# Performance work log

Measured on AMD Instinct MI355X. Metric: run time of the kernel, lower is better.

## Reference

```python
import jax, jax.numpy as jnp
import numpy as np

DIM = 768
N_HEADS = 12
HEAD_DIM = DIM // N_HEADS
B, S = 16, 1024


def setup_inputs() -> dict:
    key = jax.random.key(0)
    k1, k2, k3, k4, k5 = jax.random.split(key, 5)
    scale = 0.02
    return {
        "x": jax.random.normal(k1, (B, S, DIM), dtype=jnp.float32),
        "W_attn": jax.random.normal(k2, (DIM, 3 * DIM), dtype=jnp.float32) * scale,
        "b_attn": jnp.zeros((3 * DIM,), dtype=jnp.float32),
        "W_proj": jax.random.normal(k3, (DIM, DIM), dtype=jnp.float32) * scale,
        "b_proj": jnp.zeros((DIM,), dtype=jnp.float32),
    }


def reference(x, W_attn, b_attn, W_proj, b_proj):
    # Dropout layers act as identity (eval mode) for a deterministic reference.
    Bsz, Sq, D = x.shape
    qkv = x @ W_attn + b_attn                      # [B, S, 3D]
    q, k, v = jnp.split(qkv, 3, axis=-1)
    q = q.reshape(Bsz, Sq, N_HEADS, HEAD_DIM)
    k = k.reshape(Bsz, Sq, N_HEADS, HEAD_DIM)
    v = v.reshape(Bsz, Sq, N_HEADS, HEAD_DIM)
    # scores: [B, H, S, S]
    w = jnp.einsum('bqhd,bkhd->bhqk', q, k) / jnp.sqrt(jnp.float32(HEAD_DIM))
    causal = jnp.tril(jnp.ones((Sq, Sq), dtype=bool))
    mask_value = jnp.finfo(w.dtype).min
    w = jnp.where(causal[None, None], w, mask_value)
    w = jax.nn.softmax(w, axis=-1)
    attn = jnp.einsum('bhqk,bkhd->bqhd', w, v).reshape(Bsz, Sq, D)
    return attn @ W_proj + b_proj
```

## Files before the change

### kernel.cpp

```cpp
#include <hip/hip_runtime.h>
#include <hip/hip_bf16.h>
#include <math.h>

#define BDIM 16
#define SEQ 1024
#define DIM 768
#define NH 12
#define HD 64
#define M_ROWS (BDIM * SEQ)
#define N_QKV (3 * DIM)
#define QN (BDIM * NH * SEQ * HD)

typedef __attribute__((ext_vector_type(8))) short bf16x8_t;
typedef __attribute__((ext_vector_type(4))) float f32x4_t;
typedef __attribute__((ext_vector_type(16))) float f32x16_t;
typedef __attribute__((ext_vector_type(4))) unsigned int u32x4_t;

__device__ __forceinline__ unsigned short f2bf(float x) {
    return __builtin_bit_cast(unsigned short, __float2bfloat16(x));
}

__device__ __forceinline__ void gld_lds16(const void* g, void* l) {
    __builtin_amdgcn_global_load_lds(
        (const __attribute__((address_space(1))) void*)g,
        (__attribute__((address_space(3))) void*)l, 16, 0, 0);
}

__device__ __forceinline__ unsigned int cvt_pk_bf16(float a, float b) {
    unsigned int r;
    asm("v_cvt_pk_bf16_f32 %0, %1, %2" : "=v"(r) : "v"(a), "v"(b));
    return r;
}

__device__ __forceinline__ void perm32swap(unsigned int& a, unsigned int& b) {
    asm("v_permlane32_swap_b32 %0, %1" : "+v"(a), "+v"(b));
}

__device__ __forceinline__ float exp2_fast(float x) {
    float r;
    asm("v_exp_f32 %0, %1" : "=v"(r) : "v"(x));
    return r;
}

__device__ __forceinline__ int xcd_remap(int lin, int chunk) {
    return (lin & 7) * chunk + (lin >> 3);
}

#define QSCALE 0.18033688011112042f

#define X_BLOCKS 6144
#define WA_TILES 432
#define WP_TILES 144

__global__ __launch_bounds__(256) void prep(
    const float* __restrict__ x, const float* __restrict__ Wa,
    const float* __restrict__ Wp,
    unsigned short* __restrict__ xb, unsigned short* __restrict__ Wat,
    unsigned short* __restrict__ Wpt)
{
    __shared__ unsigned short T[64][72];
    const int bid = blockIdx.x;
    const int tid = threadIdx.x;

    if (bid < X_BLOCKS) {
        size_t base = (size_t)bid * 2048 + tid * 8;
        float4 f0 = *(const float4*)&x[base];
        float4 f1 = *(const float4*)&x[base + 4];
        unsigned short tmp[8] = {f2bf(f0.x), f2bf(f0.y), f2bf(f0.z), f2bf(f0.w),
                                 f2bf(f1.x), f2bf(f1.y), f2bf(f1.z), f2bf(f1.w)};
        *(uint4*)&xb[base] = *(uint4*)tmp;
        return;
    }
    const float* W; unsigned short* Wt; int N, kt, nt;
    int b2 = bid - X_BLOCKS;
    if (b2 < WA_TILES) { W = Wa; Wt = Wat; N = N_QKV; kt = b2 / 36; nt = b2 % 36; }
    else { b2 -= WA_TILES; W = Wp; Wt = Wpt; N = DIM; kt = b2 / 12; nt = b2 % 12; }
    const int k0 = kt * 64, n0 = nt * 64;
#pragma unroll
    for (int c = 0; c < 4; c++) {
        int idx = c * 256 + tid;
        int r = idx >> 4;
        int c4 = (idx & 15) * 4;
        float4 v = *(const float4*)&W[(size_t)(k0 + r) * N + n0 + c4];
        T[r][c4 + 0] = f2bf(v.x);
        T[r][c4 + 1] = f2bf(v.y);
        T[r][c4 + 2] = f2bf(v.z);
        T[r][c4 + 3] = f2bf(v.w);
    }
    __syncthreads();
#pragma unroll
    for (int c = 0; c < 2; c++) {
        int idx = c * 256 + tid;
        int n = idx >> 3;
        int ch = (idx & 7) * 8;
        unsigned short tmp[8];
#pragma unroll
        for (int j = 0; j < 8; j++) tmp[j] = T[ch + j][n];
        *(uint4*)&Wt[(size_t)(n0 + n) * DIM + k0 + ch] = *(uint4*)tmp;
    }
}

__global__ __launch_bounds__(256, 2) void gemm_qkv_mfma(
    const unsigned short* __restrict__ Ab,
    const unsigned short* __restrict__ Bt,
    const float* __restrict__ bias,
    unsigned short* __restrict__ Qo, unsigned short* __restrict__ Ko,
    unsigned short* __restrict__ Vt)
{
    __shared__ unsigned short smem[32768];

    const int tid = threadIdx.x;
    const int lane = tid & 63;
    const int w = tid >> 6;
    const int wm = w >> 1, wn = w & 1;
    const int ln = lane & 15, quad = lane >> 4;
    const int lin = blockIdx.x + 18 * blockIdx.y;
    const int jj = xcd_remap(lin, 288);
    const int bm = (jj / 18) * 128, bn = (jj % 18) * 128;

    f32x4_t acc[4][4];
#pragma unroll
    for (int i = 0; i < 4; i++)
#pragma unroll
        for (int j = 0; j < 4; j++) acc[i][j] = (f32x4_t){0.f, 0.f, 0.f, 0.f};

#pragma unroll
    for (int c = 0; c < 4; c++) {
        int idx = c * 256 + tid;
        int r = idx >> 3;
        int gch = (idx & 7) ^ (r & 7);
        gld_lds16(&Ab[(size_t)(bm + r) * DIM + gch * 8], &smem[idx * 8]);
        gld_lds16(&Bt[(size_t)(bn + r) * DIM + gch * 8], &smem[8192 + idx * 8]);
    }

    for (int ki = 0; ki < 12; ki++) {
        __syncthreads();
        unsigned short* As = smem + (ki & 1) * 16384;
        unsigned short* Bs = As + 8192;

        if (ki < 11) {
            const int nk0 = (ki + 1) * 64;
            unsigned short* Asn = smem + ((ki + 1) & 1) * 16384;
            unsigned short* Bsn = Asn + 8192;
#pragma unroll
            for (int c = 0; c < 4; c++) {
                int idx = c * 256 + tid;
                int r = idx >> 3;
                int gch = (idx & 7) ^ (r & 7);
                gld_lds16(&Ab[(size_t)(bm + r) * DIM + nk0 + gch * 8], &Asn[idx * 8]);
                gld_lds16(&Bt[(size_t)(bn + r) * DIM + nk0 + gch * 8], &Bsn[idx * 8]);
            }
        }

#pragma unroll
        for (int kk = 0; kk < 2; kk++) {
            bf16x8_t af[4], bfr[4];
#pragma unroll
            for (int mt = 0; mt < 4; mt++) {
                int r = wm * 64 + mt * 16 + ln;
                int c = (kk * 4 + quad) ^ (ln & 7);
                af[mt] = *(const bf16x8_t*)&As[r * 64 + c * 8];
            }
#pragma unroll
            for (int nt = 0; nt < 4; nt++) {
                int r = wn * 64 + nt * 16 + ln;
                int c = (kk * 4 + quad) ^ (ln & 7);
                bfr[nt] = *(const bf16x8_t*)&Bs[r * 64 + c * 8];
            }
#pragma unroll
            for (int mt = 0; mt < 4; mt++)
#pragma unroll
                for (int nt = 0; nt < 4; nt++)
                    acc[mt][nt] = __builtin_amdgcn_mfma_f32_16x16x32_bf16(
                        af[mt], bfr[nt], acc[mt][nt], 0, 0, 0);
        }
    }
    __syncthreads();

    const int nb = bn + wn * 64;
    const int part = nb / DIM;
    const int h = (nb % DIM) >> 6;
    const float scale = (part == 0) ? QSCALE : 1.0f;
    const int mb = bm + wm * 64;
    const int b_ = mb >> 10;
    const int s0 = mb & 1023;
    unsigned short* Wb = smem + w * 4608;

    float bias_v[4];
#pragma unroll
    for (int nt = 0; nt < 4; nt++) bias_v[nt] = bias[nb + nt * 16 + ln];

    if (part < 2) {
#pragma unroll
        for (int mt = 0; mt < 4; mt++)
#pragma unroll
            for (int nt = 0; nt < 4; nt++)
#pragma unroll
                for (int r = 0; r < 4; r++)
                    Wb[(mt * 16 + quad * 4 + r) * 72 + nt * 16 + ln] =
                        f2bf((acc[mt][nt][r] + bias_v[nt]) * scale);
        unsigned short* dst = (part == 0) ? Qo : Ko;
        size_t obase = (((size_t)b_ * NH + h) * SEQ + s0) * HD;
#pragma unroll
        for (int c = 0; c < 8; c++) {
            int idx = c * 64 + lane;
            int rr = idx >> 3;
            int ch = (idx & 7) * 8;
            *(uint4*)&dst[obase + (size_t)rr * HD + ch] = *(uint4*)&Wb[rr * 72 + ch];
        }
    } else {
#pragma unroll
        for (int mt = 0; mt < 4; mt++)
#pragma unroll
            for (int nt = 0; nt < 4; nt++)
#pragma unroll
                for (int r = 0; r < 4; r++)
                    Wb[(nt * 16 + ln) * 72 + mt * 16 + quad * 4 + r] =
                        f2bf(acc[mt][nt][r] + bias_v[nt]);
        size_t obase = ((size_t)b_ * NH + h) * (size_t)HD * SEQ;
#pragma unroll
        for (int c = 0; c < 8; c++) {
            int idx = c * 64 + lane;
            int d = idx >> 3;
            int ch = (idx & 7) * 8;
            *(uint4*)&Vt[obase + (size_t)d * SEQ + s0 + ch] = *(uint4*)&Wb[d * 72 + ch];
        }
    }
}

__global__ __launch_bounds__(256, 2) void gemm_proj_mfma(
    const unsigned short* __restrict__ Ab,
    const unsigned short* __restrict__ Bt,
    const float* __restrict__ bias,
    float* __restrict__ C)
{
    __shared__ unsigned short smem[32768];

    const int tid = threadIdx.x;
    const int lane = tid & 63;
    const int w = tid >> 6;
    const int wm = w >> 1, wn = w & 1;
    const int ln = lane & 15, quad = lane >> 4;
    const int lin = blockIdx.x + 6 * blockIdx.y;
    const int jj = xcd_remap(lin, 96);
    const int bm = (jj / 6) * 128, bn = (jj % 6) * 128;

    f32x4_t acc[4][4];
#pragma unroll
    for (int i = 0; i < 4; i++)
#pragma unroll
        for (int j = 0; j < 4; j++) acc[i][j] = (f32x4_t){0.f, 0.f, 0.f, 0.f};

#pragma unroll
    for (int c = 0; c < 4; c++) {
        int idx = c * 256 + tid;
        int r = idx >> 3;
        int gch = (idx & 7) ^ (r & 7);
        gld_lds16(&Ab[(size_t)(bm + r) * DIM + gch * 8], &smem[idx * 8]);
        gld_lds16(&Bt[(size_t)(bn + r) * DIM + gch * 8], &smem[8192 + idx * 8]);
    }

    for (int ki = 0; ki < 12; ki++) {
        __syncthreads();
        unsigned short* As = smem + (ki & 1) * 16384;
        unsigned short* Bs = As + 8192;

        if (ki < 11) {
            const int nk0 = (ki + 1) * 64;
            unsigned short* Asn = smem + ((ki + 1) & 1) * 16384;
            unsigned short* Bsn = Asn + 8192;
#pragma unroll
            for (int c = 0; c < 4; c++) {
                int idx = c * 256 + tid;
                int r = idx >> 3;
                int gch = (idx & 7) ^ (r & 7);
                gld_lds16(&Ab[(size_t)(bm + r) * DIM + nk0 + gch * 8], &Asn[idx * 8]);
                gld_lds16(&Bt[(size_t)(bn + r) * DIM + nk0 + gch * 8], &Bsn[idx * 8]);
            }
        }

#pragma unroll
        for (int kk = 0; kk < 2; kk++) {
            bf16x8_t af[4], bfr[4];
#pragma unroll
            for (int mt = 0; mt < 4; mt++) {
                int r = wm * 64 + mt * 16 + ln;
                int c = (kk * 4 + quad) ^ (ln & 7);
                af[mt] = *(const bf16x8_t*)&As[r * 64 + c * 8];
            }
#pragma unroll
            for (int nt = 0; nt < 4; nt++) {
                int r = wn * 64 + nt * 16 + ln;
                int c = (kk * 4 + quad) ^ (ln & 7);
                bfr[nt] = *(const bf16x8_t*)&Bs[r * 64 + c * 8];
            }
#pragma unroll
            for (int mt = 0; mt < 4; mt++)
#pragma unroll
                for (int nt = 0; nt < 4; nt++)
                    acc[mt][nt] = __builtin_amdgcn_mfma_f32_16x16x32_bf16(
                        af[mt], bfr[nt], acc[mt][nt], 0, 0, 0);
        }
    }

    const int nb = bn + wn * 64;
    float bias_v[4];
#pragma unroll
    for (int nt = 0; nt < 4; nt++) bias_v[nt] = bias[nb + nt * 16 + ln];
#pragma unroll
    for (int mt = 0; mt < 4; mt++)
#pragma unroll
        for (int nt = 0; nt < 4; nt++)
#pragma unroll
            for (int r = 0; r < 4; r++) {
                int m = bm + wm * 64 + mt * 16 + quad * 4 + r;
                C[(size_t)m * DIM + nb + nt * 16 + ln] = acc[mt][nt][r] + bias_v[nt];
            }
}

#define SWZ(r) ((((r) & 7)) ^ ((((r) >> 3)) & 3))

__global__ __launch_bounds__(256, 3) void attn_mfma(
    const unsigned short* __restrict__ Qg, const unsigned short* __restrict__ Kg,
    const unsigned short* __restrict__ Vt, unsigned short* __restrict__ Out)
{
    __shared__ unsigned short Ks[2][4096];
    __shared__ unsigned short Vs[2][4096];

    const int tid = threadIdx.x;
    const int lane = tid & 63;
    const int w = tid >> 6;
    const int wpair = w >> 1;
    const int whigh = w & 1;
    const int l31 = lane & 31;
    const int hi = lane >> 5;
    const int l7 = lane & 7;
    const int sw3 = (l31 >> 3) & 3;

    const int lin = blockIdx.x + 4 * blockIdx.y;
    const int jj = xcd_remap(lin, 96);
    const int bxn = jj & 3;
    const int bh = jj >> 2;
    const size_t gbase = (size_t)bh * SEQ * HD;
    const int b_ = bh / NH;
    const int h = bh % NH;

    bf16x8_t vones;
#pragma unroll
    for (int i = 0; i < 8; i++) vones[i] = (short)0x3F80;

    for (int ph = 0; ph < 2; ph++) {
        const int qt = ph ? bxn : 7 - bxn;
        const int qbase = qt * 128;
        const int ntiles = 2 * qt + 2;
        const int wtiles = 2 * qt + 1 + wpair;
        const int qr0 = qbase + w * 32;

        bf16x8_t aq[4];
#pragma unroll
        for (int ds = 0; ds < 4; ds++)
            aq[ds] = *(const bf16x8_t*)
                &Qg[gbase + (size_t)(qr0 + l31) * HD + ds * 16 + hi * 8];

        f32x16_t acc[2];
        f32x16_t lacc;
#pragma unroll
        for (int j = 0; j < 16; j++) {
            acc[0][j] = 0.f; acc[1][j] = 0.f; lacc[j] = 0.f;
        }

        __syncthreads();

#pragma unroll
        for (int i = 0; i < 2; i++) {
            int idx = i * 256 + tid;
            int r = idx >> 3;
            int gc = (idx & 7) ^ SWZ(r);
            gld_lds16(&Kg[gbase + (size_t)r * HD + gc * 8], &Ks[0][idx * 8]);
            gld_lds16(&Vt[gbase + (size_t)r * SEQ + gc * 8], &Vs[0][idx * 8]);
        }

        for (int t = 0; t < ntiles; t++) {
            __syncthreads();
            const int cur = t & 1;

            if (t + 1 < ntiles) {
                const int nk0 = (t + 1) * 64;
#pragma unroll
                for (int i = 0; i < 2; i++) {
                    int idx = i * 256 + tid;
                    int r = idx >> 3;
                    int gc = (idx & 7) ^ SWZ(r);
                    gld_lds16(&Kg[gbase + (size_t)(nk0 + r) * HD + gc * 8],
                              &Ks[cur ^ 1][idx * 8]);
                    gld_lds16(&Vt[gbase + (size_t)r * SEQ + nk0 + gc * 8],
                              &Vs[cur ^ 1][idx * 8]);
                }
            }
            if (t >= wtiles) continue;
            const bool diag = (t == 2 * qt + wpair);
            const int kgend = diag ? (1 + whigh) : 2;

            for (int kg = 0; kg < kgend; kg++) {
                bf16x8_t kf[4];
#pragma unroll
                for (int ds = 0; ds < 4; ds++)
                    kf[ds] = *(const bf16x8_t*)
                        &Ks[cur][(kg * 32 + l31) * 64 +
                                 (((ds * 2 + hi) ^ l7 ^ sw3) * 8)];

                f32x16_t sa;
#pragma unroll
                for (int j = 0; j < 16; j++) sa[j] = 0.f;
                __builtin_amdgcn_s_setprio(1);
#pragma unroll
                for (int ds = 0; ds < 4; ds++)
                    sa = __builtin_amdgcn_mfma_f32_32x32x16_bf16(
                        kf[ds], aq[ds], sa, 0, 0, 0);
                __builtin_amdgcn_s_setprio(0);

                const bool dm = diag && (kg == whigh);
                const int qr = qr0 + l31;
                float p[16];
#pragma unroll
                for (int j = 0; j < 16; j++) {
                    float pv = exp2_fast(sa[j]);
                    if (dm) {
                        int key = t * 64 + kg * 32 + (j & 3) + 8 * (j >> 2) + 4 * hi;
                        if (key > qr) pv = 0.f;
                    }
                    p[j] = pv;
                }
                unsigned int c0 = cvt_pk_bf16(p[0], p[1]);
                unsigned int c1 = cvt_pk_bf16(p[2], p[3]);
                unsigned int c2 = cvt_pk_bf16(p[4], p[5]);
                unsigned int c3 = cvt_pk_bf16(p[6], p[7]);
                unsigned int c4 = cvt_pk_bf16(p[8], p[9]);
                unsigned int c5 = cvt_pk_bf16(p[10], p[11]);
                unsigned int c6 = cvt_pk_bf16(p[12], p[13]);
                unsigned int c7 = cvt_pk_bf16(p[14], p[15]);
                perm32swap(c0, c2);
                perm32swap(c1, c3);
                perm32swap(c4, c6);
                perm32swap(c5, c7);
                u32x4_t u0, u1;
                u0[0] = c0; u0[1] = c1; u0[2] = c2; u0[3] = c3;
                u1[0] = c4; u1[1] = c5; u1[2] = c6; u1[3] = c7;
                bf16x8_t pa0 = __builtin_bit_cast(bf16x8_t, u0);
                bf16x8_t pa1 = __builtin_bit_cast(bf16x8_t, u1);

                __builtin_amdgcn_s_setprio(1);
                lacc = __builtin_amdgcn_mfma_f32_32x32x16_bf16(
                    pa0, vones, lacc, 0, 0, 0);
                lacc = __builtin_amdgcn_mfma_f32_32x32x16_bf16(
                    pa1, vones, lacc, 0, 0, 0);
#pragma unroll
                for (int dh = 0; dh < 2; dh++) {
                    bf16x8_t vf0 = *(const bf16x8_t*)
                        &Vs[cur][(dh * 32 + l31) * 64 +
                                 (((kg * 4 + 0 + hi) ^ l7 ^ sw3) * 8)];
                    acc[dh] = __builtin_amdgcn_mfma_f32_32x32x16_bf16(
                        pa0, vf0, acc[dh], 0, 0, 0);
                    bf16x8_t vf1 = *(const bf16x8_t*)
                        &Vs[cur][(dh * 32 + l31) * 64 +
                                 (((kg * 4 + 2 + hi) ^ l7 ^ sw3) * 8)];
                    acc[dh] = __builtin_amdgcn_mfma_f32_32x32x16_bf16(
                        pa1, vf1, acc[dh], 0, 0, 0);
                }
                __builtin_amdgcn_s_setprio(0);
            }
        }

        float rin[16];
#pragma unroll
        for (int j = 0; j < 16; j++) rin[j] = 1.0f / lacc[j];
#pragma unroll
        for (int dh = 0; dh < 2; dh++)
#pragma unroll
            for (int j = 0; j < 16; j++) {
                int row = qr0 + (j & 3) + 8 * (j >> 2) + 4 * hi;
                Out[((size_t)b_ * SEQ + row) * DIM + h * HD + dh * 32 + l31] =
                    f2bf(acc[dh][j] * rin[j]);
            }
    }
}

extern "C" void kernel_launch(void* const* d_in, const int* in_sizes, int n_in,
                              void* d_out, int out_size, void* d_ws, size_t ws_size,
                              hipStream_t stream) {
    const float* x  = (const float*)d_in[0];
    const float* Wa = (const float*)d_in[1];
    const float* ba = (const float*)d_in[2];
    const float* Wp = (const float*)d_in[3];
    const float* bp = (const float*)d_in[4];
    float* out = (float*)d_out;

    unsigned short* ws = (unsigned short*)d_ws;
    unsigned short* Qg  = ws;
    unsigned short* Kg  = Qg + (size_t)QN;
    unsigned short* Vt  = Kg + (size_t)QN;
    unsigned short* xb  = Vt + (size_t)QN;
    unsigned short* AO  = xb;
    unsigned short* Wat = xb + (size_t)QN;
    unsigned short* Wpt = Wat + (size_t)(N_QKV * DIM);

    prep<<<X_BLOCKS + WA_TILES + WP_TILES, 256, 0, stream>>>(
        x, Wa, Wp, xb, Wat, Wpt);

    dim3 g_qkv(N_QKV / 128, M_ROWS / 128);
    gemm_qkv_mfma<<<g_qkv, 256, 0, stream>>>(xb, Wat, ba, Qg, Kg, Vt);

    dim3 g_attn(4, BDIM * NH);
    attn_mfma<<<g_attn, 256, 0, stream>>>(Qg, Kg, Vt, AO);

    dim3 g_proj(DIM / 128, M_ROWS / 128);
    gemm_proj_mfma<<<g_proj, 256, 0, stream>>>(AO, Wpt, bp, out);
}
```

Baseline: 239.0 us.

## Enlarge GEMM tiles to 256x256 with 512 threads and deeper prefetch

Both the QKV and projection GEMMs move from 128x128 tiles with 4 waves to 256x256 tiles with 8 waves. Each wave now computes a 128x64 sub-tile, and B fragments are reused across four A sub-steps. Loads are issued two K-steps ahead, using explicit vmcnt waits and s_setprio around the MFMA bursts. This raises data reuse per byte loaded but cuts the grid to 72 and 24 blocks on a many-CU GPU, and the larger LDS footprint limits occupancy.

```diff
diff --git a/kernel.cpp b/kernel.cpp
--- a/kernel.cpp
+++ b/kernel.cpp
@@ -100,206 +100,235 @@
     }
 }
 
-__global__ __launch_bounds__(256, 2) void gemm_qkv_mfma(
+__device__ __forceinline__ void stage_tile256(
+    const unsigned short* __restrict__ Ab, const unsigned short* __restrict__ Bt,
+    int bm, int bn, int k0, unsigned short* Asd, unsigned short* Bsd, int tid)
+{
+#pragma unroll
+    for (int rr = 0; rr < 4; rr++) {
+        int idx = rr * 512 + tid;
+        int r = idx >> 3;
+        int gch = (idx & 7) ^ (r & 7);
+        gld_lds16(&Ab[(size_t)(bm + r) * DIM + k0 + gch * 8], &Asd[idx * 8]);
+    }
+#pragma unroll
+    for (int rr = 0; rr < 4; rr++) {
+        int idx = rr * 512 + tid;
+        int r = idx >> 3;
+        int gch = (idx & 7) ^ (r & 7);
+        gld_lds16(&Bt[(size_t)(bn + r) * DIM + k0 + gch * 8], &Bsd[idx * 8]);
+    }
+}
+
+__global__ __launch_bounds__(512, 2) void gemm_qkv_mfma(
     const unsigned short* __restrict__ Ab,
     const unsigned short* __restrict__ Bt,
     const float* __restrict__ bias,
     unsigned short* __restrict__ Qo, unsigned short* __restrict__ Ko,
     unsigned short* __restrict__ Vt)
 {
-    __shared__ unsigned short smem[32768];
+    __shared__ unsigned short As[2 * 16384];
+    __shared__ unsigned short Bs[2 * 16384];
 
     const int tid = threadIdx.x;
     const int lane = tid & 63;
     const int w = tid >> 6;
-    const int wm = w >> 1, wn = w & 1;
+    const int wm = w >> 2, wn = w & 3;
     const int ln = lane & 15, quad = lane >> 4;
-    const int lin = blockIdx.x + 18 * blockIdx.y;
-    const int jj = xcd_remap(lin, 288);
-    const int bm = (jj / 18) * 128, bn = (jj % 18) * 128;
-
-    f32x4_t acc[4][4];
-#pragma unroll
-    for (int i = 0; i < 4; i++)
+
+    const int lin = blockIdx.x + 9 * blockIdx.y;
+    const int jj = xcd_remap(lin, 72);
+    const int bm = (jj / 9) * 256, bn = (jj % 9) * 256;
+
+    f32x4_t acc[8][4];
+#pragma unroll
+    for (int i = 0; i < 8; i++)
 #pragma unroll
         for (int j = 0; j < 4; j++) acc[i][j] = (f32x4_t){0.f, 0.f, 0.f, 0.f};
 
-#pragma unroll
-    for (int c = 0; c < 4; c++) {
-        int idx = c * 256 + tid;
-        int r = idx >> 3;
-        int gch = (idx & 7) ^ (r & 7);
-        gld_lds16(&Ab[(size_t)(bm + r) * DIM + gch * 8], &smem[idx * 8]);
-        gld_lds16(&Bt[(size_t)(bn + r) * DIM + gch * 8], &smem[8192 + idx * 8]);
-    }
-
-    for (int ki = 0; ki < 12; ki++) {
-        __syncthreads();
-        unsigned short* As = smem + (ki & 1) * 16384;
-        unsigned short* Bs = As + 8192;
-
-        if (ki < 11) {
-            const int nk0 = (ki + 1) * 64;
-            unsigned short* Asn = smem + ((ki + 1) & 1) * 16384;
-            unsigned short* Bsn = Asn + 8192;
-#pragma unroll
-            for (int c = 0; c < 4; c++) {
-                int idx = c * 256 + tid;
-                int r = idx >> 3;
-                int gch = (idx & 7) ^ (r & 7);
-                gld_lds16(&Ab[(size_t)(bm + r) * DIM + nk0 + gch * 8], &Asn[idx * 8]);
-                gld_lds16(&Bt[(size_t)(bn + r) * DIM + nk0 + gch * 8], &Bsn[idx * 8]);
-            }
-        }
-
-#pragma unroll
-        for (int kk = 0; kk < 2; kk++) {
-            bf16x8_t af[4], bfr[4];
-#pragma unroll
-            for (int mt = 0; mt < 4; mt++) {
-                int r = wm * 64 + mt * 16 + ln;
-                int c = (kk * 4 + quad) ^ (ln & 7);
-                af[mt] = *(const bf16x8_t*)&As[r * 64 + c * 8];
-            }
-#pragma unroll
-            for (int nt = 0; nt < 4; nt++) {
+    stage_tile256(Ab, Bt, bm, bn, 0, As, Bs, tid);
+    stage_tile256(Ab, Bt, bm, bn, 64, As + 16384, Bs + 16384, tid);
+    asm volatile("s_waitcnt vmcnt(8)" ::: "memory");
+    __syncthreads();
+
+    for (int k = 0; k < 12; k++) {
+        const unsigned short* As_ = As + (k & 1) * 16384;
+        const unsigned short* Bs_ = Bs + (k & 1) * 16384;
+
+        bf16x8_t bfr[4][2];
+#pragma unroll
+        for (int nt = 0; nt < 4; nt++)
+#pragma unroll
+            for (int kk = 0; kk < 2; kk++) {
                 int r = wn * 64 + nt * 16 + ln;
                 int c = (kk * 4 + quad) ^ (ln & 7);
-                bfr[nt] = *(const bf16x8_t*)&Bs[r * 64 + c * 8];
-            }
-#pragma unroll
-            for (int mt = 0; mt < 4; mt++)
+                bfr[nt][kk] = *(const bf16x8_t*)&Bs_[r * 64 + c * 8];
+            }
+#pragma unroll
+        for (int q = 0; q < 4; q++) {
+            bf16x8_t af[2][2];
+#pragma unroll
+            for (int mi = 0; mi < 2; mi++)
+#pragma unroll
+                for (int kk = 0; kk < 2; kk++) {
+                    int r = wm * 128 + (q * 2 + mi) * 16 + ln;
+                    int c = (kk * 4 + quad) ^ (ln & 7);
+                    af[mi][kk] = *(const bf16x8_t*)&As_[r * 64 + c * 8];
+                }
+            __builtin_amdgcn_s_setprio(1);
+#pragma unroll
+            for (int mi = 0; mi < 2; mi++)
 #pragma unroll
                 for (int nt = 0; nt < 4; nt++)
-                    acc[mt][nt] = __builtin_amdgcn_mfma_f32_16x16x32_bf16(
-                        af[mt], bfr[nt], acc[mt][nt], 0, 0, 0);
-        }
-    }
-    __syncthreads();
+#pragma unroll
+                    for (int kk = 0; kk < 2; kk++)
+                        acc[q * 2 + mi][nt] = __builtin_amdgcn_mfma_f32_16x16x32_bf16(
+                            af[mi][kk], bfr[nt][kk], acc[q * 2 + mi][nt], 0, 0, 0);
+            __builtin_amdgcn_s_setprio(0);
+        }
+
+        __syncthreads();
+        if (k + 2 < 12)
+            stage_tile256(Ab, Bt, bm, bn, (k + 2) * 64,
+                          (unsigned short*)As + (k & 1) * 16384,
+                          (unsigned short*)Bs + (k & 1) * 16384, tid);
+        if (k + 1 < 12) {
+            if (k + 2 < 12) asm volatile("s_waitcnt vmcnt(8)" ::: "memory");
+            else            asm volatile("s_waitcnt vmcnt(0)" ::: "memory");
+            __syncthreads();
+        }
+    }
 
     const int nb = bn + wn * 64;
     const int part = nb / DIM;
     const int h = (nb % DIM) >> 6;
     const float scale = (part == 0) ? QSCALE : 1.0f;
-    const int mb = bm + wm * 64;
+    const int mb = bm + wm * 128;
     const int b_ = mb >> 10;
     const int s0 = mb & 1023;
-    unsigned short* Wb = smem + w * 4608;
+    unsigned short* Wb = (w < 4) ? (As + w * 4608) : (Bs + (w - 4) * 4608);
 
     float bias_v[4];
 #pragma unroll
     for (int nt = 0; nt < 4; nt++) bias_v[nt] = bias[nb + nt * 16 + ln];
 
-    if (part < 2) {
-#pragma unroll
-        for (int mt = 0; mt < 4; mt++)
-#pragma unroll
-            for (int nt = 0; nt < 4; nt++)
-#pragma unroll
-                for (int r = 0; r < 4; r++)
-                    Wb[(mt * 16 + quad * 4 + r) * 72 + nt * 16 + ln] =
-                        f2bf((acc[mt][nt][r] + bias_v[nt]) * scale);
-        unsigned short* dst = (part == 0) ? Qo : Ko;
-        size_t obase = (((size_t)b_ * NH + h) * SEQ + s0) * HD;
-#pragma unroll
-        for (int c = 0; c < 8; c++) {
-            int idx = c * 64 + lane;
-            int rr = idx >> 3;
-            int ch = (idx & 7) * 8;
-            *(uint4*)&dst[obase + (size_t)rr * HD + ch] = *(uint4*)&Wb[rr * 72 + ch];
-        }
-    } else {
-#pragma unroll
-        for (int mt = 0; mt < 4; mt++)
-#pragma unroll
-            for (int nt = 0; nt < 4; nt++)
-#pragma unroll
-                for (int r = 0; r < 4; r++)
-                    Wb[(nt * 16 + ln) * 72 + mt * 16 + quad * 4 + r] =
-                        f2bf(acc[mt][nt][r] + bias_v[nt]);
-        size_t obase = ((size_t)b_ * NH + h) * (size_t)HD * SEQ;
-#pragma unroll
-        for (int c = 0; c < 8; c++) {
-            int idx = c * 64 + lane;
-            int d = idx >> 3;
-            int ch = (idx & 7) * 8;
-            *(uint4*)&Vt[obase + (size_t)d * SEQ + s0 + ch] = *(uint4*)&Wb[d * 72 + ch];
-        }
-    }
-}
-
-__global__ __launch_bounds__(256, 2) void gemm_proj_mfma(
+#pragma unroll
+    for (int g = 0; g < 2; g++) {
+        if (part < 2) {
+#pragma unroll
+            for (int lt = 0; lt < 4; lt++)
+#pragma unroll
+                for (int nt = 0; nt < 4; nt++)
+#pragma unroll
+                    for (int r = 0; r < 4; r++)
+                        Wb[(lt * 16 + quad * 4 + r) * 72 + nt * 16 + ln] =
+                            f2bf((acc[g * 4 + lt][nt][r] + bias_v[nt]) * scale);
+            unsigned short* dst = (part == 0) ? Qo : Ko;
+            size_t obase = (((size_t)b_ * NH + h) * SEQ + s0 + g * 64) * HD;
+#pragma unroll
+            for (int c = 0; c < 8; c++) {
+                int idx = c * 64 + lane;
+                int rr = idx >> 3;
+                int ch = (idx & 7) * 8;
+                *(uint4*)&dst[obase + (size_t)rr * HD + ch] = *(uint4*)&Wb[rr * 72 + ch];
+            }
+        } else {
+#pragma unroll
+            for (int lt = 0; lt < 4; lt++)
+#pragma unroll
+                for (int nt = 0; nt < 4; nt++)
+#pragma unroll
+                    for (int r = 0; r < 4; r++)
+                        Wb[(nt * 16 + ln) * 72 + lt * 16 + quad * 4 + r] =
+                            f2bf(acc[g * 4 + lt][nt][r] + bias_v[nt]);
+            size_t obase = ((size_t)b_ * NH + h) * (size_t)HD * SEQ;
+#pragma unroll
+            for (int c = 0; c < 8; c++) {
+                int idx = c * 64 + lane;
+                int d = idx >> 3;
+                int ch = (idx & 7) * 8;
+                *(uint4*)&Vt[obase + (size_t)d * SEQ + s0 + g * 64 + ch] =
+                    *(uint4*)&Wb[d * 72 + ch];
+            }
+        }
+    }
+}
+
+__global__ __launch_bounds__(512, 2) void gemm_proj_mfma(
     const unsigned short* __restrict__ Ab,
     const unsigned short* __restrict__ Bt,
     const float* __restrict__ bias,
     float* __restrict__ C)
 {
-    __shared__ unsigned short smem[32768];
+    __shared__ unsigned short As[2 * 16384];
+    __shared__ unsigned short Bs[2 * 16384];
 
     const int tid = threadIdx.x;
     const int lane = tid & 63;
     const int w = tid >> 6;
-    const int wm = w >> 1, wn = w & 1;
+    const int wm = w >> 2, wn = w & 3;
     const int ln = lane & 15, quad = lane >> 4;
-    const int lin = blockIdx.x + 6 * blockIdx.y;
-    const int jj = xcd_remap(lin, 96);
-    const int bm = (jj / 6) * 128, bn = (jj % 6) * 128;
-
-    f32x4_t acc[4][4];
-#pragma unroll
-    for (int i = 0; i < 4; i++)
+
+    const int lin = blockIdx.x + 3 * blockIdx.y;
+    const int jj = xcd_remap(lin, 24);
+    const int bm = (jj / 3) * 256, bn = (jj % 3) * 256;
+
+    f32x4_t acc[8][4];
+#pragma unroll
+    for (int i = 0; i < 8; i++)
 #pragma unroll
         for (int j = 0; j < 4; j++) acc[i][j] = (f32x4_t){0.f, 0.f, 0.f, 0.f};
 
-#pragma unroll
-    for (int c = 0; c < 4; c++) {
-        int idx = c * 256 + tid;
-        int r = idx >> 3;
-        int gch = (idx & 7) ^ (r & 7);
-        gld_lds16(&Ab[(size_t)(bm + r) * DIM + gch * 8], &smem[idx * 8]);
-        gld_lds16(&Bt[(size_t)(bn + r) * DIM + gch * 8], &smem[8192 + idx * 8]);
-    }
-
-    for (int ki = 0; ki < 12; ki++) {
-        __syncthreads();
-        unsigned short* As = smem + (ki & 1) * 16384;
-        unsigned short* Bs = As + 8192;
-
-        if (ki < 11) {
-            const int nk0 = (ki + 1) * 64;
-            unsigned short* Asn = smem + ((ki + 1) & 1) * 16384;
-            unsigned short* Bsn = Asn + 8192;
-#pragma unroll
-            for (int c = 0; c < 4; c++) {
-                int idx = c * 256 + tid;
-                int r = idx >> 3;
-                int gch = (idx & 7) ^ (r & 7);
-                gld_lds16(&Ab[(size_t)(bm + r) * DIM + nk0 + gch * 8], &Asn[idx * 8]);
-                gld_lds16(&Bt[(size_t)(bn + r) * DIM + nk0 + gch * 8], &Bsn[idx * 8]);
-            }
-        }
-
-#pragma unroll
-        for (int kk = 0; kk < 2; kk++) {
-            bf16x8_t af[4], bfr[4];
-#pragma unroll
-            for (int mt = 0; mt < 4; mt++) {
-                int r = wm * 64 + mt * 16 + ln;
-                int c = (kk * 4 + quad) ^ (ln & 7);
-                af[mt] = *(const bf16x8_t*)&As[r * 64 + c * 8];
-            }
-#pragma unroll
-            for (int nt = 0; nt < 4; nt++) {
+    stage_tile256(Ab, Bt, bm, bn, 0, As, Bs, tid);
+    stage_tile256(Ab, Bt, bm, bn, 64, As + 16384, Bs + 16384, tid);
+    asm volatile("s_waitcnt vmcnt(8)" ::: "memory");
+    __syncthreads();
+
+    for (int k = 0; k < 12; k++) {
+        const unsigned short* As_ = As + (k & 1) * 16384;
+        const unsigned short* Bs_ = Bs + (k & 1) * 16384;
+
+        bf16x8_t bfr[4][2];
+#pragma unroll
+        for (int nt = 0; nt < 4; nt++)
+#pragma unroll
+            for (int kk = 0; kk < 2; kk++) {
                 int r = wn * 64 + nt * 16 + ln;
                 int c = (kk * 4 + quad) ^ (ln & 7);
-                bfr[nt] = *(const bf16x8_t*)&Bs[r * 64 + c * 8];
-            }
-#pragma unroll
-            for (int mt = 0; mt < 4; mt++)
+                bfr[nt][kk] = *(const bf16x8_t*)&Bs_[r * 64 + c * 8];
+            }
+#pragma unroll
+        for (int q = 0; q < 4; q++) {
+            bf16x8_t af[2][2];
+#pragma unroll
+            for (int mi = 0; mi < 2; mi++)
+#pragma unroll
+                for (int kk = 0; kk < 2; kk++) {
+                    int r = wm * 128 + (q * 2 + mi) * 16 + ln;
+                    int c = (kk * 4 + quad) ^ (ln & 7);
+                    af[mi][kk] = *(const bf16x8_t*)&As_[r * 64 + c * 8];
+                }
+            __builtin_amdgcn_s_setprio(1);
+#pragma unroll
+            for (int mi = 0; mi < 2; mi++)
 #pragma unroll
                 for (int nt = 0; nt < 4; nt++)
-                    acc[mt][nt] = __builtin_amdgcn_mfma_f32_16x16x32_bf16(
-                        af[mt], bfr[nt], acc[mt][nt], 0, 0, 0);
+#pragma unroll
+                    for (int kk = 0; kk < 2; kk++)
+                        acc[q * 2 + mi][nt] = __builtin_amdgcn_mfma_f32_16x16x32_bf16(
+                            af[mi][kk], bfr[nt][kk], acc[q * 2 + mi][nt], 0, 0, 0);
+            __builtin_amdgcn_s_setprio(0);
+        }
+
+        __syncthreads();
+        if (k + 2 < 12)
+            stage_tile256(Ab, Bt, bm, bn, (k + 2) * 64,
+                          (unsigned short*)As + (k & 1) * 16384,
+                          (unsigned short*)Bs + (k & 1) * 16384, tid);
+        if (k + 1 < 12) {
+            if (k + 2 < 12) asm volatile("s_waitcnt vmcnt(8)" ::: "memory");
+            else            asm volatile("s_waitcnt vmcnt(0)" ::: "memory");
+            __syncthreads();
         }
     }
 
@@ -308,12 +337,12 @@
 #pragma unroll
     for (int nt = 0; nt < 4; nt++) bias_v[nt] = bias[nb + nt * 16 + ln];
 #pragma unroll
-    for (int mt = 0; mt < 4; mt++)
+    for (int mt = 0; mt < 8; mt++)
 #pragma unroll
         for (int nt = 0; nt < 4; nt++)
 #pragma unroll
             for (int r = 0; r < 4; r++) {
-                int m = bm + wm * 64 + mt * 16 + quad * 4 + r;
+                int m = bm + wm * 128 + mt * 16 + quad * 4 + r;
                 C[(size_t)m * DIM + nb + nt * 16 + ln] = acc[mt][nt][r] + bias_v[nt];
             }
 }
@@ -507,12 +536,12 @@
     prep<<<X_BLOCKS + WA_TILES + WP_TILES, 256, 0, stream>>>(
         x, Wa, Wp, xb, Wat, Wpt);
 
-    dim3 g_qkv(N_QKV / 128, M_ROWS / 128);
-    gemm_qkv_mfma<<<g_qkv, 256, 0, stream>>>(xb, Wat, ba, Qg, Kg, Vt);
+    dim3 g_qkv(N_QKV / 256, M_ROWS / 256);
+    gemm_qkv_mfma<<<g_qkv, 512, 0, stream>>>(xb, Wat, ba, Qg, Kg, Vt);
 
     dim3 g_attn(4, BDIM * NH);
     attn_mfma<<<g_attn, 256, 0, stream>>>(Qg, Kg, Vt, AO);
 
-    dim3 g_proj(DIM / 128, M_ROWS / 128);
-    gemm_proj_mfma<<<g_proj, 256, 0, stream>>>(AO, Wpt, bp, out);
-}
+    dim3 g_proj(DIM / 256, M_ROWS / 256);
+    gemm_proj_mfma<<<g_proj, 512, 0, stream>>>(AO, Wpt, bp, out);
+}
```

After: 273.1 us. 14.3% more time.

## Deepen GEMM prefetch to two tiles ahead with partial vmcnt waits

Applied to the files above, without the earlier changes.

Both the QKV and output-projection GEMMs now keep two K-tiles of global-to-LDS loads in flight. Each iteration waits only for the older batch through a partial vmcnt count, and uses explicit barriers and sched_barriers in place of __syncthreads, which drained all outstanding loads. MFMA blocks are also wrapped in s_setprio to favour the compute wave. This is meant to hide global load latency behind MFMA work. The cost is hand-managed synchronisation that depends on the exact per-thread load count.

```diff
diff --git a/kernel.cpp b/kernel.cpp
--- a/kernel.cpp
+++ b/kernel.cpp
@@ -100,6 +100,20 @@
     }
 }
 
+__device__ __forceinline__ void stage_tile128(
+    const unsigned short* __restrict__ Ab, const unsigned short* __restrict__ Bt,
+    int bm, int bn, int k0, unsigned short* buf, int tid)
+{
+#pragma unroll
+    for (int c = 0; c < 4; c++) {
+        int idx = c * 256 + tid;
+        int r = idx >> 3;
+        int gch = (idx & 7) ^ (r & 7);
+        gld_lds16(&Ab[(size_t)(bm + r) * DIM + k0 + gch * 8], &buf[idx * 8]);
+        gld_lds16(&Bt[(size_t)(bn + r) * DIM + k0 + gch * 8], &buf[8192 + idx * 8]);
+    }
+}
+
 __global__ __launch_bounds__(256, 2) void gemm_qkv_mfma(
     const unsigned short* __restrict__ Ab,
     const unsigned short* __restrict__ Bt,
@@ -124,33 +138,16 @@
 #pragma unroll
         for (int j = 0; j < 4; j++) acc[i][j] = (f32x4_t){0.f, 0.f, 0.f, 0.f};
 
-#pragma unroll
-    for (int c = 0; c < 4; c++) {
-        int idx = c * 256 + tid;
-        int r = idx >> 3;
-        int gch = (idx & 7) ^ (r & 7);
-        gld_lds16(&Ab[(size_t)(bm + r) * DIM + gch * 8], &smem[idx * 8]);
-        gld_lds16(&Bt[(size_t)(bn + r) * DIM + gch * 8], &smem[8192 + idx * 8]);
-    }
+    stage_tile128(Ab, Bt, bm, bn, 0, smem, tid);
+    stage_tile128(Ab, Bt, bm, bn, 64, smem + 16384, tid);
+    asm volatile("s_waitcnt vmcnt(8)" ::: "memory");
+    __builtin_amdgcn_sched_barrier(0);
+    __builtin_amdgcn_s_barrier();
+    __builtin_amdgcn_sched_barrier(0);
 
     for (int ki = 0; ki < 12; ki++) {
-        __syncthreads();
-        unsigned short* As = smem + (ki & 1) * 16384;
-        unsigned short* Bs = As + 8192;
-
-        if (ki < 11) {
-            const int nk0 = (ki + 1) * 64;
-            unsigned short* Asn = smem + ((ki + 1) & 1) * 16384;
-            unsigned short* Bsn = Asn + 8192;
-#pragma unroll
-            for (int c = 0; c < 4; c++) {
-                int idx = c * 256 + tid;
-                int r = idx >> 3;
-                int gch = (idx & 7) ^ (r & 7);
-                gld_lds16(&Ab[(size_t)(bm + r) * DIM + nk0 + gch * 8], &Asn[idx * 8]);
-                gld_lds16(&Bt[(size_t)(bn + r) * DIM + nk0 + gch * 8], &Bsn[idx * 8]);
-            }
-        }
+        const unsigned short* As = smem + (ki & 1) * 16384;
+        const unsigned short* Bs = As + 8192;
 
 #pragma unroll
         for (int kk = 0; kk < 2; kk++) {
@@ -167,12 +164,29 @@
                 int c = (kk * 4 + quad) ^ (ln & 7);
                 bfr[nt] = *(const bf16x8_t*)&Bs[r * 64 + c * 8];
             }
+            __builtin_amdgcn_s_setprio(1);
 #pragma unroll
             for (int mt = 0; mt < 4; mt++)
 #pragma unroll
                 for (int nt = 0; nt < 4; nt++)
                     acc[mt][nt] = __builtin_amdgcn_mfma_f32_16x16x32_bf16(
                         af[mt], bfr[nt], acc[mt][nt], 0, 0, 0);
+            __builtin_amdgcn_s_setprio(0);
+        }
+
+        if (ki < 11) {
+            __builtin_amdgcn_s_barrier();
+            __builtin_amdgcn_sched_barrier(0);
+            if (ki < 10) {
+                stage_tile128(Ab, Bt, bm, bn, (ki + 2) * 64,
+                              smem + (ki & 1) * 16384, tid);
+                asm volatile("s_waitcnt vmcnt(8)" ::: "memory");
+            } else {
+                asm volatile("s_waitcnt vmcnt(0)" ::: "memory");
+            }
+            __builtin_amdgcn_sched_barrier(0);
+            __builtin_amdgcn_s_barrier();
+            __builtin_amdgcn_sched_barrier(0);
         }
     }
     __syncthreads();
@@ -251,33 +265,16 @@
 #pragma unroll
         for (int j = 0; j < 4; j++) acc[i][j] = (f32x4_t){0.f, 0.f, 0.f, 0.f};
 
-#pragma unroll
-    for (int c = 0; c < 4; c++) {
-        int idx = c * 256 + tid;
-        int r = idx >> 3;
-        int gch = (idx & 7) ^ (r & 7);
-        gld_lds16(&Ab[(size_t)(bm + r) * DIM + gch * 8], &smem[idx * 8]);
-        gld_lds16(&Bt[(size_t)(bn + r) * DIM + gch * 8], &smem[8192 + idx * 8]);
-    }
+    stage_tile128(Ab, Bt, bm, bn, 0, smem, tid);
+    stage_tile128(Ab, Bt, bm, bn, 64, smem + 16384, tid);
+    asm volatile("s_waitcnt vmcnt(8)" ::: "memory");
+    __builtin_amdgcn_sched_barrier(0);
+    __builtin_amdgcn_s_barrier();
+    __builtin_amdgcn_sched_barrier(0);
 
     for (int ki = 0; ki < 12; ki++) {
-        __syncthreads();
-        unsigned short* As = smem + (ki & 1) * 16384;
-        unsigned short* Bs = As + 8192;
-
-        if (ki < 11) {
-            const int nk0 = (ki + 1) * 64;
-            unsigned short* Asn = smem + ((ki + 1) & 1) * 16384;
-            unsigned short* Bsn = Asn + 8192;
-#pragma unroll
-            for (int c = 0; c < 4; c++) {
-                int idx = c * 256 + tid;
-                int r = idx >> 3;
-                int gch = (idx & 7) ^ (r & 7);
-                gld_lds16(&Ab[(size_t)(bm + r) * DIM + nk0 + gch * 8], &Asn[idx * 8]);
-                gld_lds16(&Bt[(size_t)(bn + r) * DIM + nk0 + gch * 8], &Bsn[idx * 8]);
-            }
-        }
+        const unsigned short* As = smem + (ki & 1) * 16384;
+        const unsigned short* Bs = As + 8192;
 
 #pragma unroll
         for (int kk = 0; kk < 2; kk++) {
@@ -294,12 +291,29 @@
                 int c = (kk * 4 + quad) ^ (ln & 7);
                 bfr[nt] = *(const bf16x8_t*)&Bs[r * 64 + c * 8];
             }
+            __builtin_amdgcn_s_setprio(1);
 #pragma unroll
             for (int mt = 0; mt < 4; mt++)
 #pragma unroll
                 for (int nt = 0; nt < 4; nt++)
                     acc[mt][nt] = __builtin_amdgcn_mfma_f32_16x16x32_bf16(
                         af[mt], bfr[nt], acc[mt][nt], 0, 0, 0);
+            __builtin_amdgcn_s_setprio(0);
+        }
+
+        if (ki < 11) {
+            __builtin_amdgcn_s_barrier();
+            __builtin_amdgcn_sched_barrier(0);
+            if (ki < 10) {
+                stage_tile128(Ab, Bt, bm, bn, (ki + 2) * 64,
+                              smem + (ki & 1) * 16384, tid);
+                asm volatile("s_waitcnt vmcnt(8)" ::: "memory");
+            } else {
+                asm volatile("s_waitcnt vmcnt(0)" ::: "memory");
+            }
+            __builtin_amdgcn_sched_barrier(0);
+            __builtin_amdgcn_s_barrier();
+            __builtin_amdgcn_sched_barrier(0);
         }
     }
 
```

Result: no change. 242.9 us (+1.6%).
